# Kernel optimization log

Hardware: AMD Instinct MI355X
Metric: run time of the kernel (lower is better)

Reference implementation:

```python
import jax, jax.numpy as jnp
import numpy as np

N_NODES = 100000
N_EDGES = 1600000
HID = 128
BOND = 16
BN_EPS = 1e-5


def setup_inputs() -> dict:
    key = jax.random.key(0)
    ks = jax.random.split(key, 12)
    sb = 1.0 / np.sqrt(BOND)
    sh = 1.0 / np.sqrt(HID)
    return {
        "features": jax.random.normal(ks[0], (N_NODES, HID), jnp.float32),
        "edge_feats": jax.random.normal(ks[1], (N_EDGES, BOND), jnp.float32),
        "src": jax.random.randint(ks[2], (N_EDGES,), 0, N_NODES, jnp.int32),
        "dst": jax.random.randint(ks[3], (N_EDGES,), 0, N_NODES, jnp.int32),
        "Wb": jax.random.uniform(ks[4], (HID, BOND), jnp.float32, -sb, sb),
        "bb": jax.random.uniform(ks[5], (HID,), jnp.float32, -sb, sb),
        "W1": jax.random.uniform(ks[6], (HID, HID), jnp.float32, -sh, sh),
        "b1": jax.random.uniform(ks[7], (HID,), jnp.float32, -sh, sh),
        "W2": jax.random.uniform(ks[8], (HID, HID), jnp.float32, -sh, sh),
        "b2": jax.random.uniform(ks[9], (HID,), jnp.float32, -sh, sh),
        "gamma1": jnp.ones((HID,), jnp.float32),
        "beta1": jnp.zeros((HID,), jnp.float32),
        "gamma2": jnp.ones((HID,), jnp.float32),
        "beta2": jnp.zeros((HID,), jnp.float32),
    }


def _batchnorm(x, gamma, beta):
    # BatchNorm1d in training mode: normalize with batch stats (biased var).
    mean = jnp.mean(x, axis=0)
    var = jnp.var(x, axis=0)
    return (x - mean) * jax.lax.rsqrt(var + BN_EPS) * gamma + beta


def reference(features, edge_feats, src, dst, Wb, bb, W1, b1, W2, b2,
              gamma1, beta1, gamma2, beta2):
    n = features.shape[0]
    # edge linear: [E, BOND] -> [E, HID]
    eh = edge_feats @ Wb.T + bb
    # mailbox sums: sum of src node features and edge messages per dst node
    h1 = jax.ops.segment_sum(features[src], dst, num_segments=n)  # [N, HID]
    h2 = jax.ops.segment_sum(eh, dst, num_segments=n)             # [N, HID]
    h = jax.nn.relu(_batchnorm(h1 @ W1.T + b1 + h2, gamma1, beta1))
    h = jax.nn.relu(_batchnorm(h @ W2.T + b2 + features, gamma2, beta2))
    return h
```

## Files before the change

kernel.cpp:

```cpp
#include <hip/hip_runtime.h>

#define NN 100000
#define NE 1600000
#define HID 128
#define KEXT 160
#define ROWB 320
#define BSH 9
#define BNODES 512
#define NB 196
#define P2B 1024
#define EPB2 1563
#define SCAP 10240
#define NROWP 100096
#define GGRID 782
#define BN_EPS 1e-5f

typedef __attribute__((ext_vector_type(8))) short bf16x8;
typedef __attribute__((ext_vector_type(4))) float f32x4;

__device__ inline unsigned short f2bf(float x) {
  union { float f; unsigned u; } v; v.f = x;
  unsigned r = v.u + 0x7FFFu + ((v.u >> 16) & 1u);
  return (unsigned short)(r >> 16);
}
__device__ inline unsigned pk2(float a, float b) {
  return (unsigned)f2bf(a) | ((unsigned)f2bf(b) << 16);
}
__device__ inline float bflo(unsigned p) { return __uint_as_float(p << 16); }
__device__ inline float bfhi(unsigned p) { return __uint_as_float(p & 0xffff0000u); }

__device__ inline void gload_lds16(const void* g, void* l) {
  __builtin_amdgcn_global_load_lds((const __attribute__((address_space(1))) void*)g,
                                   (__attribute__((address_space(3))) void*)l, 16, 0, 0);
}

__global__ __launch_bounds__(256) void fbw_k(const float* __restrict__ f,
                                             unsigned* __restrict__ fb,
                                             const float* __restrict__ W1,
                                             const float* __restrict__ Wb,
                                             const float* __restrict__ bb,
                                             const float* __restrict__ b1,
                                             const float* __restrict__ W2,
                                             unsigned short* __restrict__ W1e,
                                             unsigned short* __restrict__ W2e,
                                             const int* __restrict__ dst,
                                             int* __restrict__ cnts_s) {
  __shared__ int bh[NB];
  if (blockIdx.x < 25000) {
    int i = blockIdx.x * 256 + threadIdx.x;
    float2 v = ((const float2*)f)[i];
    fb[i] = pk2(v.x, v.y);
  } else if (blockIdx.x < 25080) {
    int idx = (blockIdx.x - 25000) * 256 + threadIdx.x;
    if (idx < 128 * KEXT) {
      int c = idx / KEXT, k = idx - c * KEXT;
      float v1 = 0.f;
      if (k < 128) v1 = W1[c * HID + k];
      else if (k < 144) v1 = Wb[c * 16 + (k - 128)];
      else if (k == 144) v1 = bb[c];
      else if (k == 145) v1 = b1[c];
      W1e[idx] = f2bf(v1);
    }
    if (idx < 128 * 128) W2e[idx] = f2bf(W2[(idx >> 7) * HID + (idx & 127)]);
  } else {
    int blk = blockIdx.x - 25080;
    int b0 = blk * EPB2, e1 = min(b0 + EPB2, NE);
    for (int i = threadIdx.x; i < NB; i += 256) bh[i] = 0;
    __syncthreads();
    for (int e = b0 + threadIdx.x; e < e1; e += 256) atomicAdd(&bh[dst[e] >> BSH], 1);
    __syncthreads();
    for (int i = threadIdx.x; i < NB; i += 256) cnts_s[i * P2B + blk] = bh[i];
  }
}

__global__ __launch_bounds__(P2B) void cscan_k(int* __restrict__ cnts_s,
                                               int* __restrict__ bcnt_s,
                                               int* __restrict__ bcnt_r) {
  __shared__ int s[P2B];
  int b = blockIdx.x, t = threadIdx.x;
  int x = cnts_s[b * P2B + t];
  int xs = (x + 7) & ~7;
  s[t] = xs; __syncthreads();
  for (int off = 1; off < P2B; off <<= 1) {
    int v = (t >= off) ? s[t - off] : 0; __syncthreads();
    s[t] += v; __syncthreads();
  }
  cnts_s[b * P2B + t] = s[t] - xs;
  if (t == P2B - 1) bcnt_s[b] = s[t];
  __syncthreads();
  s[t] = x; __syncthreads();
  for (int off = 1; off < P2B; off <<= 1) {
    int v = (t >= off) ? s[t - off] : 0; __syncthreads();
    s[t] += v; __syncthreads();
  }
  if (t == P2B - 1) bcnt_r[b] = s[t];
}

__global__ __launch_bounds__(256) void bscan_k(const int* __restrict__ bcnt_r,
                                               const int* __restrict__ bcnt_s,
                                               int* __restrict__ bbase_r,
                                               int* __restrict__ bbase_s,
                                               int* __restrict__ rs) {
  __shared__ int s[256];
  int t = threadIdx.x;
#pragma unroll
  for (int pass = 0; pass < 2; ++pass) {
    const int* in = (pass == 0) ? bcnt_r : bcnt_s;
    int* out = (pass == 0) ? bbase_r : bbase_s;
    int x = (t < NB) ? in[t] : 0;
    s[t] = x; __syncthreads();
    for (int off = 1; off < 256; off <<= 1) {
      int v = (t >= off) ? s[t - off] : 0; __syncthreads();
      s[t] += v; __syncthreads();
    }
    if (t < NB) out[t] = s[t] - x;
    if (t == NB - 1) out[NB] = s[t];
    __syncthreads();
  }
  if (t == 0) rs[NN] = NE;
}

__global__ __launch_bounds__(256) void part3_k(const int* __restrict__ src,
                                               const int* __restrict__ dst,
                                               const float* __restrict__ ef,
                                               const int* __restrict__ bbase_s,
                                               const int* __restrict__ cnts_s,
                                               unsigned* __restrict__ stg,
                                               float4* __restrict__ efb) {
  __shared__ int th[NB], ts[NB], cnt2[NB], st_s[NB];
  __shared__ int sscan[256];
  __shared__ unsigned spk[EPB2 + 1];
  int blk = blockIdx.x, tid = threadIdx.x;
  int b0 = blk * EPB2;
  int tc = min(EPB2, NE - b0);
  for (int i = tid; i < NB; i += 256) {
    th[i] = 0; cnt2[i] = 0;
    st_s[i] = bbase_s[i] + cnts_s[i * P2B + blk];
  }
  __syncthreads();
  float sink = 0.f;
  for (int le = tid; le < tc; le += 256) {
    int e = b0 + le;
    atomicAdd(&th[dst[e] >> BSH], 1);
    const float4* efp = (const float4*)(ef + (size_t)e * 16);
    float4 a = efp[0], b4 = efp[1], c4 = efp[2], d4 = efp[3];
    sink += a.x + b4.x + c4.x + d4.x;
  }
  asm volatile("" : "+v"(sink));
  __syncthreads();
  sscan[tid] = (tid < NB) ? th[tid] : 0;
  __syncthreads();
  for (int off = 1; off < 256; off <<= 1) {
    int v = (tid >= off) ? sscan[tid - off] : 0;
    __syncthreads();
    sscan[tid] += v;
    __syncthreads();
  }
  if (tid < NB) ts[tid] = sscan[tid] - th[tid];
  __syncthreads();
  for (int le = tid; le < tc; le += 256) {
    int d = dst[b0 + le];
    int b = d >> BSH;
    int slot = ts[b] + atomicAdd(&cnt2[b], 1);
    spk[slot] = ((unsigned)b << 20) | ((unsigned)(d & (BNODES - 1)) << 11) | (unsigned)le;
  }
  __syncthreads();
  for (int s2 = tid; s2 < tc; s2 += 256) {
    unsigned pk = spk[s2];
    int b = pk >> 20, d9 = (pk >> 11) & 511, le = pk & 2047;
    int e = b0 + le;
    int gs = st_s[b] + (s2 - ts[b]);
    stg[gs] = (unsigned)src[e] | ((unsigned)d9 << 17) | (1u << 26);
    const float4* efp = (const float4*)(ef + (size_t)e * 16);
    float4 a = efp[0], b4 = efp[1], c4 = efp[2], d4 = efp[3];
    float4 w0, w1;
    w0.x = __uint_as_float(pk2(a.x, a.y));   w0.y = __uint_as_float(pk2(a.z, a.w));
    w0.z = __uint_as_float(pk2(b4.x, b4.y)); w0.w = __uint_as_float(pk2(b4.z, b4.w));
    w1.x = __uint_as_float(pk2(c4.x, c4.y)); w1.y = __uint_as_float(pk2(c4.z, c4.w));
    w1.z = __uint_as_float(pk2(d4.x, d4.y)); w1.w = __uint_as_float(pk2(d4.z, d4.w));
    efb[(size_t)gs * 2] = w0;
    efb[(size_t)gs * 2 + 1] = w1;
  }
  __syncthreads();
  for (int i = tid; i < NB; i += 256) {
    int c = th[i];
    int cs = (c + 7) & ~7;
    for (int j = c; j < cs; ++j) stg[st_s[i] + j] = 0u;
  }
}

__global__ __launch_bounds__(512) void bsort_k(const unsigned* __restrict__ stg,
                                               const int* __restrict__ bbase_s,
                                               const int* __restrict__ bbase_r,
                                               const unsigned* __restrict__ efbu,
                                               int* __restrict__ rs,
                                               unsigned* __restrict__ fin,
                                               unsigned* __restrict__ efsum) {
  __shared__ int h[BNODES], sc[BNODES], cur[BNODES];
  __shared__ int tot;
  __shared__ unsigned slds[SCAP];
  int b = blockIdx.x, n0 = b << BSH, tid = threadIdx.x;
  int s0p = bbase_s[b], e1p = bbase_s[b + 1];
  int s0r = bbase_r[b];
  h[tid] = 0;
  __syncthreads();
  for (int i = s0p + tid; i < e1p; i += 512) {
    unsigned rec = stg[i];
    if (rec >> 26) atomicAdd(&h[(rec >> 17) & (BNODES - 1)], 1);
  }
  __syncthreads();
  sc[tid] = h[tid];
  __syncthreads();
  for (int off = 1; off < BNODES; off <<= 1) {
    int v = (tid >= off) ? sc[tid - off] : 0;
    __syncthreads();
    sc[tid] += v;
    __syncthreads();
  }
  int excl = sc[tid] - h[tid];
  cur[tid] = excl;
  int n = n0 + tid;
  if (n < NN) rs[n] = s0r + excl;
  if (tid == BNODES - 1) tot = sc[tid];
  __syncthreads();
  for (int i = s0p + tid; i < e1p; i += 512) {
    unsigned rec = stg[i];
    if (rec >> 26) {
      int d = (rec >> 17) & (BNODES - 1);
      int p = atomicAdd(&cur[d], 1);
      slds[p] = (rec & 0x1FFFF) | ((unsigned)(i - s0p) << 17);
    }
  }
  __syncthreads();
  int T = tot;
  for (int j = tid; j < T; j += 512) fin[s0r + j] = slds[j] & 0x1FFFF;
  if (n < NN) {
    float a[16];
#pragma unroll
    for (int k = 0; k < 16; ++k) a[k] = 0.f;
    for (int j = excl; j < sc[tid]; ++j) {
      unsigned rec = slds[j];
      const unsigned* ep = efbu + ((size_t)s0p + (rec >> 17)) * 8;
#pragma unroll
      for (int k = 0; k < 8; ++k) {
        unsigned u = ep[k];
        a[2 * k] += bflo(u);
        a[2 * k + 1] += bfhi(u);
      }
    }
    unsigned* op = efsum + (size_t)n * 8;
#pragma unroll
    for (int k = 0; k < 8; ++k) op[k] = pk2(a[2 * k], a[2 * k + 1]);
  }
}

__global__ __launch_bounds__(256) void feg_k(const unsigned* __restrict__ fb,
                                             const int* __restrict__ rs,
                                             const unsigned* __restrict__ fin,
                                             const unsigned* __restrict__ efsum,
                                             unsigned short* __restrict__ A1) {
  int bid = (int)(blockIdx.x & 7) * 3125 + (int)(blockIdx.x >> 3);
  int wid = threadIdx.x >> 6, lane = threadIdx.x & 63;
  int node = bid * 4 + wid;
  if (node >= NN) return;
  int start = rs[node], end = rs[node + 1];
  float ax0 = 0.f, ay0 = 0.f, ax1 = 0.f, ay1 = 0.f;
  float ax2 = 0.f, ay2 = 0.f, ax3 = 0.f, ay3 = 0.f;
  float ax4 = 0.f, ay4 = 0.f, ax5 = 0.f, ay5 = 0.f;
  float ax6 = 0.f, ay6 = 0.f, ax7 = 0.f, ay7 = 0.f;
  int i = start;
  for (; i + 8 <= end; i += 8) {
    int sl = 0;
    if (lane < 8) sl = (int)fin[i + lane];
    int s0 = __shfl(sl, 0), s1 = __shfl(sl, 1), s2 = __shfl(sl, 2), s3 = __shfl(sl, 3);
    int s4 = __shfl(sl, 4), s5 = __shfl(sl, 5), s6 = __shfl(sl, 6), s7 = __shfl(sl, 7);
    unsigned p0 = fb[s0 * 64 + lane];
    unsigned p1 = fb[s1 * 64 + lane];
    unsigned p2 = fb[s2 * 64 + lane];
    unsigned p3 = fb[s3 * 64 + lane];
    unsigned p4 = fb[s4 * 64 + lane];
    unsigned p5 = fb[s5 * 64 + lane];
    unsigned p6 = fb[s6 * 64 + lane];
    unsigned p7 = fb[s7 * 64 + lane];
    ax0 += bflo(p0); ay0 += bfhi(p0);
    ax1 += bflo(p1); ay1 += bfhi(p1);
    ax2 += bflo(p2); ay2 += bfhi(p2);
    ax3 += bflo(p3); ay3 += bfhi(p3);
    ax4 += bflo(p4); ay4 += bfhi(p4);
    ax5 += bflo(p5); ay5 += bfhi(p5);
    ax6 += bflo(p6); ay6 += bfhi(p6);
    ax7 += bflo(p7); ay7 += bfhi(p7);
  }
  for (; i < end; ++i) {
    int sl = 0;
    if (lane == 0) sl = (int)fin[i];
    int s0 = __shfl(sl, 0);
    unsigned p0 = fb[s0 * 64 + lane];
    ax0 += bflo(p0); ay0 += bfhi(p0);
  }
  float ax = ((ax0 + ax1) + (ax2 + ax3)) + ((ax4 + ax5) + (ax6 + ax7));
  float ay = ((ay0 + ay1) + (ay2 + ay3)) + ((ay4 + ay5) + (ay6 + ay7));
  char* rowp = (char*)A1 + (size_t)node * ROWB;
  *(unsigned*)(rowp + lane * 4) = pk2(ax, ay);
  if (lane < 8) {
    *(unsigned*)(rowp + 256 + 4 * lane) = efsum[(size_t)node * 8 + lane];
  } else if (lane < 16) {
    int j2 = lane - 8;
    *(unsigned*)(rowp + 288 + 4 * j2) =
        (j2 == 0) ? pk2((float)(end - start), 1.0f) : 0u;
  }
}

__global__ __launch_bounds__(256) void gemm1_k(
    const unsigned short* __restrict__ A, const unsigned short* __restrict__ W,
    unsigned short* __restrict__ outb, float* __restrict__ statsP) {
  __shared__ __align__(16) char sA[128 * ROWB];
  __shared__ __align__(16) char sW[128 * ROWB];
  const int tid = threadIdx.x;
  const int wid = tid >> 6, lane = tid & 63;
  const size_t r0 = (size_t)blockIdx.x * 128;

#pragma unroll
  for (int q = 0; q < 10; ++q) {
    int s = q * 256 + tid;
    int row = (s * 3277) >> 16;
    int c = s - row * 20;
    int csrc = (c < 16) ? (c ^ (row & 7)) : (16 + ((c - 16) ^ (row & 3)));
    gload_lds16((const char*)A + (r0 + row) * ROWB + csrc * 16,
                sA + (size_t)(q * 256 + wid * 64) * 16);
  }
#pragma unroll
  for (int q = 0; q < 10; ++q) {
    int s = q * 256 + tid;
    int row = (s * 3277) >> 16;
    int c = s - row * 20;
    int csrc = (c < 16) ? (c ^ (row & 7)) : (16 + ((c - 16) ^ (row & 3)));
    gload_lds16((const char*)W + (size_t)row * ROWB + csrc * 16,
                sW + (size_t)(q * 256 + wid * 64) * 16);
  }
  __syncthreads();

  const int l15 = lane & 15;
  const int kgr = lane >> 4;
  bf16x8 afrag[2][5];
#pragma unroll
  for (int rt = 0; rt < 2; ++rt) {
    int arow = wid * 32 + rt * 16 + l15;
#pragma unroll
    for (int ks = 0; ks < 5; ++ks) {
      int creq = ks * 4 + kgr;
      int csw = (creq < 16) ? (creq ^ (arow & 7)) : (16 + ((creq - 16) ^ (arow & 3)));
      afrag[rt][ks] = *(const bf16x8*)(sA + arow * ROWB + csw * 16);
    }
  }
  f32x4 acc[2][8];
#pragma unroll
  for (int rt = 0; rt < 2; ++rt)
#pragma unroll
    for (int ct = 0; ct < 8; ++ct) acc[rt][ct] = (f32x4){0.f, 0.f, 0.f, 0.f};
#pragma unroll
  for (int ct = 0; ct < 8; ++ct) {
    int brow = ct * 16 + l15;
#pragma unroll
    for (int ks = 0; ks < 5; ++ks) {
      int creq = ks * 4 + kgr;
      int csw = (creq < 16) ? (creq ^ (brow & 7)) : (16 + ((creq - 16) ^ (brow & 3)));
      bf16x8 bfrag = *(const bf16x8*)(sW + brow * ROWB + csw * 16);
      acc[0][ct] = __builtin_amdgcn_mfma_f32_16x16x32_bf16(afrag[0][ks], bfrag, acc[0][ct], 0, 0, 0);
      acc[1][ct] = __builtin_amdgcn_mfma_f32_16x16x32_bf16(afrag[1][ks], bfrag, acc[1][ct], 0, 0, 0);
    }
  }

  float cs[8], cq[8];
#pragma unroll
  for (int ct = 0; ct < 8; ++ct) { cs[ct] = 0.f; cq[ct] = 0.f; }
#pragma unroll
  for (int rt = 0; rt < 2; ++rt) {
    const size_t orow0 = r0 + wid * 32 + rt * 16 + kgr * 4;
#pragma unroll
    for (int ct = 0; ct < 8; ++ct) {
      int col = ct * 16 + l15;
#pragma unroll
      for (int r = 0; r < 4; ++r) {
        size_t row = orow0 + r;
        if (row < NN) {
          float v = acc[rt][ct][r];
          outb[row * HID + col] = f2bf(v);
          cs[ct] += v; cq[ct] += v * v;
        }
      }
    }
  }
#pragma unroll
  for (int ct = 0; ct < 8; ++ct) {
    cs[ct] += __shfl_xor(cs[ct], 16); cs[ct] += __shfl_xor(cs[ct], 32);
    cq[ct] += __shfl_xor(cq[ct], 16); cq[ct] += __shfl_xor(cq[ct], 32);
  }
  __syncthreads();
  float* red = (float*)sA;
  if (lane < 16) {
#pragma unroll
    for (int ct = 0; ct < 8; ++ct) {
      red[wid * 256 + ct * 16 + l15] = cs[ct];
      red[wid * 256 + 128 + ct * 16 + l15] = cq[ct];
    }
  }
  __syncthreads();
  if (tid < 256) {
    float* base = statsP + (size_t)(blockIdx.x & 15) * 512;
    float s_ = red[tid] + red[256 + tid] + red[512 + tid] + red[768 + tid];
    atomicAdd(&base[tid], s_);
  }
}

__global__ void bnred_k(const float* __restrict__ statsP, int base,
                        const float* __restrict__ gamma, const float* __restrict__ beta,
                        float* __restrict__ scale, float* __restrict__ shift) {
  int c = threadIdx.x;
  if (c < 128) {
    float s_ = 0.f, q_ = 0.f;
#pragma unroll
    for (int i = 0; i < 16; ++i) {
      s_ += statsP[i * 512 + base + c];
      q_ += statsP[i * 512 + base + 128 + c];
    }
    const float invN = 1.f / (float)NN;
    float m = s_ * invN;
    float var = q_ * invN - m * m;
    float inv = rsqrtf(var + BN_EPS);
    float sc = gamma[c] * inv;
    scale[c] = sc;
    shift[c] = beta[c] - m * sc;
  }
}

__global__ __launch_bounds__(256) void gemm2_k(
    const unsigned* __restrict__ t, const unsigned short* __restrict__ W,
    const float* __restrict__ scale, const float* __restrict__ shift,
    const float* __restrict__ b2, const unsigned* __restrict__ fbres,
    unsigned short* __restrict__ outb, float* __restrict__ statsP) {
  __shared__ __align__(16) char sA[128 * 256];
  __shared__ __align__(16) char sW[128 * 256];
  __shared__ float ssc[128], ssh[128];
  const int tid = threadIdx.x;
  const int wid = tid >> 6, lane = tid & 63;
  const size_t r0 = (size_t)blockIdx.x * 128;

  if (tid < 128) {
    ssc[tid] = scale[tid];
    ssh[tid] = shift[tid];
  }
#pragma unroll
  for (int q = 0; q < 8; ++q) {
    int s = q * 256 + tid;
    int row = s >> 4, c = s & 15;
    int csrc = c ^ (row & 7);
    gload_lds16((const char*)W + (size_t)row * 256 + csrc * 16,
                sW + (size_t)(q * 256 + wid * 64) * 16);
  }
  __syncthreads();

#pragma unroll
  for (int q = 0; q < 8; ++q) {
    int s = q * 256 + tid;
    int sr = s >> 4, c = s & 15;
    size_t grow = r0 + sr;
    uint4 v = make_uint4(0, 0, 0, 0);
    if (grow < NN) v = *(const uint4*)(t + grow * 64 + c * 4);
    int k = c * 8;
    unsigned o0 = pk2(fmaxf(0.f, fmaf(bflo(v.x), ssc[k + 0], ssh[k + 0])),
                      fmaxf(0.f, fmaf(bfhi(v.x), ssc[k + 1], ssh[k + 1])));
    unsigned o1 = pk2(fmaxf(0.f, fmaf(bflo(v.y), ssc[k + 2], ssh[k + 2])),
                      fmaxf(0.f, fmaf(bfhi(v.y), ssc[k + 3], ssh[k + 3])));
    unsigned o2 = pk2(fmaxf(0.f, fmaf(bflo(v.z), ssc[k + 4], ssh[k + 4])),
                      fmaxf(0.f, fmaf(bfhi(v.z), ssc[k + 5], ssh[k + 5])));
    unsigned o3 = pk2(fmaxf(0.f, fmaf(bflo(v.w), ssc[k + 6], ssh[k + 6])),
                      fmaxf(0.f, fmaf(bfhi(v.w), ssc[k + 7], ssh[k + 7])));
    int csw = c ^ (sr & 7);
    uint4 w4; w4.x = o0; w4.y = o1; w4.z = o2; w4.w = o3;
    *(uint4*)(sA + sr * 256 + csw * 16) = w4;
  }
  __syncthreads();

  const int l15 = lane & 15;
  const int kgr = lane >> 4;
  bf16x8 afrag[2][4];
#pragma unroll
  for (int rt = 0; rt < 2; ++rt) {
    int arow = wid * 32 + rt * 16 + l15;
#pragma unroll
    for (int ks = 0; ks < 4; ++ks) {
      int creq = ks * 4 + kgr;
      int csw = creq ^ (arow & 7);
      afrag[rt][ks] = *(const bf16x8*)(sA + arow * 256 + csw * 16);
    }
  }
  f32x4 acc[2][8];
#pragma unroll
  for (int rt = 0; rt < 2; ++rt)
#pragma unroll
    for (int ct = 0; ct < 8; ++ct) acc[rt][ct] = (f32x4){0.f, 0.f, 0.f, 0.f};
#pragma unroll
  for (int ct = 0; ct < 8; ++ct) {
    int brow = ct * 16 + l15;
#pragma unroll
    for (int ks = 0; ks < 4; ++ks) {
      int creq = ks * 4 + kgr;
      int csw = creq ^ (brow & 7);
      bf16x8 bfrag = *(const bf16x8*)(sW + brow * 256 + csw * 16);
      acc[0][ct] = __builtin_amdgcn_mfma_f32_16x16x32_bf16(afrag[0][ks], bfrag, acc[0][ct], 0, 0, 0);
      acc[1][ct] = __builtin_amdgcn_mfma_f32_16x16x32_bf16(afrag[1][ks], bfrag, acc[1][ct], 0, 0, 0);
    }
  }

  float cs[8], cq[8];
#pragma unroll
  for (int ct = 0; ct < 8; ++ct) { cs[ct] = 0.f; cq[ct] = 0.f; }
#pragma unroll
  for (int rt = 0; rt < 2; ++rt) {
    const size_t orow0 = r0 + wid * 32 + rt * 16 + kgr * 4;
#pragma unroll
    for (int ct = 0; ct < 8; ++ct) {
      int col = ct * 16 + l15;
      float b2v = b2[col];
      int ci = col >> 1, par = col & 1;
#pragma unroll
      for (int r = 0; r < 4; ++r) {
        size_t row = orow0 + r;
        if (row < NN) {
          unsigned u = fbres[row * 64 + ci];
          float resid = par ? bfhi(u) : bflo(u);
          float v = acc[rt][ct][r] + b2v + resid;
          outb[row * HID + col] = f2bf(v);
          cs[ct] += v; cq[ct] += v * v;
        }
      }
    }
  }
#pragma unroll
  for (int ct = 0; ct < 8; ++ct) {
    cs[ct] += __shfl_xor(cs[ct], 16); cs[ct] += __shfl_xor(cs[ct], 32);
    cq[ct] += __shfl_xor(cq[ct], 16); cq[ct] += __shfl_xor(cq[ct], 32);
  }
  __syncthreads();
  float* red = (float*)sA;
  if (lane < 16) {
#pragma unroll
    for (int ct = 0; ct < 8; ++ct) {
      red[wid * 256 + ct * 16 + l15] = cs[ct];
      red[wid * 256 + 128 + ct * 16 + l15] = cq[ct];
    }
  }
  __syncthreads();
  if (tid < 256) {
    float* base = statsP + (size_t)(blockIdx.x & 15) * 512 + 256;
    float s_ = red[tid] + red[256 + tid] + red[512 + tid] + red[768 + tid];
    atomicAdd(&base[tid], s_);
  }
}

__global__ __launch_bounds__(256) void bn_final_k(const unsigned* __restrict__ t,
                                                  const float* __restrict__ scale,
                                                  const float* __restrict__ shift,
                                                  float* __restrict__ o) {
  __shared__ float ssc[128], ssh[128];
  int tid = threadIdx.x;
  if (tid < 128) { ssc[tid] = scale[tid]; ssh[tid] = shift[tid]; }
  __syncthreads();
  int i = blockIdx.x * 256 + tid;
  if (i >= NN * 64) return;
  unsigned p = t[i];
  int c = (i & 63) * 2;
  float2 v;
  v.x = fmaxf(0.f, fmaf(bflo(p), ssc[c], ssh[c]));
  v.y = fmaxf(0.f, fmaf(bfhi(p), ssc[c + 1], ssh[c + 1]));
  ((float2*)o)[i] = v;
}

extern "C" void kernel_launch(void* const* d_in, const int* in_sizes, int n_in,
                              void* d_out, int out_size, void* d_ws, size_t ws_size,
                              hipStream_t stream) {
  (void)in_sizes; (void)n_in; (void)out_size; (void)ws_size;
  const float* features   = (const float*)d_in[0];
  const float* edge_feats = (const float*)d_in[1];
  const int*   src        = (const int*)d_in[2];
  const int*   dst        = (const int*)d_in[3];
  const float* Wb         = (const float*)d_in[4];
  const float* bb         = (const float*)d_in[5];
  const float* W1         = (const float*)d_in[6];
  const float* b1         = (const float*)d_in[7];
  const float* W2         = (const float*)d_in[8];
  const float* b2         = (const float*)d_in[9];
  const float* gamma1     = (const float*)d_in[10];
  const float* beta1      = (const float*)d_in[11];
  const float* gamma2     = (const float*)d_in[12];
  const float* beta2      = (const float*)d_in[13];
  float* outp = (float*)d_out;

  char* wsb = (char*)d_ws;
  size_t off = 0;
  auto alloc = [&](size_t nbytes) -> void* {
    off = (off + 255) & ~(size_t)255;
    void* p = wsb + off;
    off += nbytes;
    return p;
  };
  const size_t STGN = (size_t)NE + 7 * (size_t)NB * P2B + 64;
  int* row_start = (int*)alloc((size_t)(NN + 1) * 4);
  int* bcnt_r    = (int*)alloc(NB * 4);
  int* bcnt_s    = (int*)alloc(NB * 4);
  int* bbase_r   = (int*)alloc((NB + 1) * 4);
  int* bbase_s   = (int*)alloc((NB + 1) * 4);
  int* cnts_s    = (int*)alloc((size_t)NB * P2B * 4);
  float* statsP  = (float*)alloc(16 * 512 * 4);
  float* scsh    = (float*)alloc(512 * 4);
  unsigned* featb = (unsigned*)alloc((size_t)NN * 64 * 4);
  unsigned short* tbuf = (unsigned short*)alloc((size_t)NROWP * HID * 2);
  unsigned short* A1e = (unsigned short*)alloc((size_t)NROWP * ROWB);
  unsigned short* W1e = (unsigned short*)alloc(128 * KEXT * 2);
  unsigned short* W2e = (unsigned short*)alloc(128 * 128 * 2);
  unsigned* stg  = (unsigned*)alloc(STGN * 4);
  unsigned* fin  = (unsigned*)alloc((size_t)NE * 4);
  float4* efb    = (float4*)alloc(STGN * 32);
  unsigned* efsum = (unsigned*)alloc((size_t)NN * 32);

  hipMemsetAsync(statsP, 0, 16 * 512 * 4, stream);
  hipMemsetAsync((char*)A1e + (size_t)NN * ROWB, 0, (NROWP - NN) * ROWB, stream);

  fbw_k<<<25080 + P2B, 256, 0, stream>>>(features, featb, W1, Wb, bb, b1, W2,
                                         W1e, W2e, dst, cnts_s);
  cscan_k<<<NB, P2B, 0, stream>>>(cnts_s, bcnt_s, bcnt_r);
  bscan_k<<<1, 256, 0, stream>>>(bcnt_r, bcnt_s, bbase_r, bbase_s, row_start);
  part3_k<<<P2B, 256, 0, stream>>>(src, dst, edge_feats, bbase_s, cnts_s, stg, efb);
  bsort_k<<<NB, 512, 0, stream>>>(stg, bbase_s, bbase_r, (const unsigned*)efb,
                                  row_start, fin, efsum);
  feg_k<<<25000, 256, 0, stream>>>(featb, row_start, fin, efsum, A1e);

  gemm1_k<<<GGRID, 256, 0, stream>>>(A1e, W1e, tbuf, statsP);
  bnred_k<<<1, 128, 0, stream>>>(statsP, 0, gamma1, beta1, scsh, scsh + 128);
  gemm2_k<<<GGRID, 256, 0, stream>>>((const unsigned*)tbuf, W2e, scsh, scsh + 128,
                                     b2, featb, tbuf, statsP);
  bnred_k<<<1, 128, 0, stream>>>(statsP, 256, gamma2, beta2, scsh + 256, scsh + 384);
  bn_final_k<<<25000, 256, 0, stream>>>((const unsigned*)tbuf, scsh + 256, scsh + 384,
                                        outp);
}
```

Before: 302.5 us.

## Double edge-partition blocks and pad per-bucket staging to 2 instead of 8

Doubles the number of edge-partition blocks (2048 with about 782 edges each) so the histogram and scatter kernels spread over more workgroups. The column scan is reworked so each thread handles two entries, and per-bucket staging padding drops from a multiple of 8 to a multiple of 2. This shrinks padding entries in the staging buffer that the bucket sort must read. The catch is a larger count matrix and that any downstream code assuming 8-aligned segments (such as vectorized loads in bsort_k) must still be correct.

```diff
diff --git a/kernel.cpp b/kernel.cpp
--- a/kernel.cpp
+++ b/kernel.cpp
@@ -8,8 +8,8 @@
 #define BSH 9
 #define BNODES 512
 #define NB 196
-#define P2B 1024
-#define EPB2 1563
+#define P2B 2048
+#define EPB2 782
 #define SCAP 10240
 #define NROWP 100096
 #define GGRID 782
@@ -73,27 +73,31 @@
   }
 }
 
-__global__ __launch_bounds__(P2B) void cscan_k(int* __restrict__ cnts_s,
-                                               int* __restrict__ bcnt_s,
-                                               int* __restrict__ bcnt_r) {
-  __shared__ int s[P2B];
+__global__ __launch_bounds__(1024) void cscan_k(int* __restrict__ cnts_s,
+                                                int* __restrict__ bcnt_s,
+                                                int* __restrict__ bcnt_r) {
+  __shared__ int s[1024];
   int b = blockIdx.x, t = threadIdx.x;
-  int x = cnts_s[b * P2B + t];
-  int xs = (x + 7) & ~7;
-  s[t] = xs; __syncthreads();
-  for (int off = 1; off < P2B; off <<= 1) {
+  int x0 = cnts_s[b * P2B + 2 * t];
+  int x1 = cnts_s[b * P2B + 2 * t + 1];
+  int xs0 = (x0 + 1) & ~1;
+  int xs1 = (x1 + 1) & ~1;
+  s[t] = xs0 + xs1; __syncthreads();
+  for (int off = 1; off < 1024; off <<= 1) {
     int v = (t >= off) ? s[t - off] : 0; __syncthreads();
     s[t] += v; __syncthreads();
   }
-  cnts_s[b * P2B + t] = s[t] - xs;
-  if (t == P2B - 1) bcnt_s[b] = s[t];
-  __syncthreads();
-  s[t] = x; __syncthreads();
-  for (int off = 1; off < P2B; off <<= 1) {
+  int exclp = s[t] - (xs0 + xs1);
+  cnts_s[b * P2B + 2 * t] = exclp;
+  cnts_s[b * P2B + 2 * t + 1] = exclp + xs0;
+  if (t == 1023) bcnt_s[b] = s[1023];
+  __syncthreads();
+  s[t] = x0 + x1; __syncthreads();
+  for (int off = 1; off < 1024; off <<= 1) {
     int v = (t >= off) ? s[t - off] : 0; __syncthreads();
     s[t] += v; __syncthreads();
   }
-  if (t == P2B - 1) bcnt_r[b] = s[t];
+  if (t == 1023) bcnt_r[b] = s[1023];
 }
 
 __global__ __launch_bounds__(256) void bscan_k(const int* __restrict__ bcnt_r,
@@ -133,6 +137,7 @@
   int blk = blockIdx.x, tid = threadIdx.x;
   int b0 = blk * EPB2;
   int tc = min(EPB2, NE - b0);
+  if (tc < 0) tc = 0;
   for (int i = tid; i < NB; i += 256) {
     th[i] = 0; cnt2[i] = 0;
     st_s[i] = bbase_s[i] + cnts_s[i * P2B + blk];
@@ -184,8 +189,7 @@
   __syncthreads();
   for (int i = tid; i < NB; i += 256) {
     int c = th[i];
-    int cs = (c + 7) & ~7;
-    for (int j = c; j < cs; ++j) stg[st_s[i] + j] = 0u;
+    if (c & 1) stg[st_s[i] + c] = 0u;
   }
 }
 
@@ -605,7 +609,7 @@
     off += nbytes;
     return p;
   };
-  const size_t STGN = (size_t)NE + 7 * (size_t)NB * P2B + 64;
+  const size_t STGN = (size_t)NE + (size_t)NB * P2B + 64;
   int* row_start = (int*)alloc((size_t)(NN + 1) * 4);
   int* bcnt_r    = (int*)alloc(NB * 4);
   int* bcnt_s    = (int*)alloc(NB * 4);
@@ -629,7 +633,7 @@
 
   fbw_k<<<25080 + P2B, 256, 0, stream>>>(features, featb, W1, Wb, bb, b1, W2,
                                          W1e, W2e, dst, cnts_s);
-  cscan_k<<<NB, P2B, 0, stream>>>(cnts_s, bcnt_s, bcnt_r);
+  cscan_k<<<NB, 1024, 0, stream>>>(cnts_s, bcnt_s, bcnt_r);
   bscan_k<<<1, 256, 0, stream>>>(bcnt_r, bcnt_s, bbase_r, bbase_s, row_start);
   part3_k<<<P2B, 256, 0, stream>>>(src, dst, edge_feats, bbase_s, cnts_s, stg, efb);
   bsort_k<<<NB, 512, 0, stream>>>(stg, bbase_s, bbase_r, (const unsigned*)efb,
```

Result: faster. 292.6 us (-3.3%).
